# Kernel optimization log

Measured on AMD Instinct MI355X. Metric: run time of the kernel, lower is better.

The kernel has to match this reference:

```python
import jax, jax.numpy as jnp
import numpy as np

TEMPERATURE = 0.07
EPS = 1e-8  # torch CosineSimilarity eps default


def setup_inputs() -> dict:
    key = jax.random.key(0)
    k1, k2 = jax.random.split(key)
    N, D = 8192, 1024
    image_features = jax.random.normal(k1, (N, D), dtype=jnp.float32)
    text_features = jax.random.normal(k2, (N, D), dtype=jnp.float32)
    return {"image_features": image_features, "text_features": text_features}


def _normalize(x):
    # matches torch cosine similarity denominator clamp: norm >= eps
    n = jnp.sqrt(jnp.sum(x * x, axis=-1, keepdims=True))
    return x / jnp.maximum(n, EPS)


def reference(image_features, text_features):
    # cosine similarity via normalize + GEMM (same math as broadcasted NxNxD form)
    img_n = _normalize(image_features)  # [N, D]
    txt_n = _normalize(text_features)   # [N, D]
    logits = jnp.einsum('id,jd->ij', img_n, txt_n) / TEMPERATURE  # [N, N]

    N = logits.shape[0]
    labels = jnp.arange(N)
    # cross-entropy with labels = diagonal indices
    logp_i2t = jax.nn.log_softmax(logits, axis=-1)      # rows: image -> text
    logp_t2i = jax.nn.log_softmax(logits.T, axis=-1)    # rows: text -> image
    loss_i2t = -jnp.mean(logp_i2t[labels, labels])
    loss_t2i = -jnp.mean(logp_t2i[labels, labels])
    return (loss_i2t + loss_t2i) / 2
```

## Files before the change

### kernel.cpp

```cpp
#include <hip/hip_runtime.h>


#define BM 128
#define BN 128
#define BKB 128

typedef float floatx4 __attribute__((ext_vector_type(4)));
typedef int   intx4   __attribute__((ext_vector_type(4)));
typedef int   intx8   __attribute__((ext_vector_type(8)));

__device__ __forceinline__ void gload_lds16(const unsigned char* g, unsigned char* lds) {
    __builtin_amdgcn_global_load_lds(
        (const __attribute__((address_space(1))) void*)g,
        (__attribute__((address_space(3))) void*)lds,
        16, 0, 0);
}

__global__ __launch_bounds__(256)
void normalize_fp8(const float* __restrict__ img, const float* __restrict__ txt,
                   unsigned int* __restrict__ oimg, unsigned int* __restrict__ otxt,
                   float* __restrict__ sums, float* __restrict__ out, int N) {
    const int gi = blockIdx.x * 256 + threadIdx.x;
    if (gi < 2 * N) sums[gi] = 0.f;
    if (gi == 0) out[0] = 0.f;

    const int gw = blockIdx.x * 4 + (threadIdx.x >> 6);
    const int lane = threadIdx.x & 63;
    const float* in = (gw < N) ? img : txt;
    unsigned int* o = (gw < N) ? oimg : otxt;
    const int row = (gw < N) ? gw : gw - N;
    const float4* rp = (const float4*)(in + (size_t)row * 1024);

    float4 v[4];
    float ss = 0.f;
    #pragma unroll
    for (int j = 0; j < 4; ++j) {
        v[j] = rp[j * 64 + lane];
        ss += v[j].x * v[j].x + v[j].y * v[j].y + v[j].z * v[j].z + v[j].w * v[j].w;
    }
    #pragma unroll
    for (int o2 = 1; o2 < 64; o2 <<= 1) ss += __shfl_xor(ss, o2);
    const float inv = 16.0f / fmaxf(sqrtf(ss), 1e-8f);
    #pragma unroll
    for (int j = 0; j < 4; ++j) {
        int p = __builtin_amdgcn_cvt_pk_fp8_f32(v[j].x * inv, v[j].y * inv, 0, false);
        p = __builtin_amdgcn_cvt_pk_fp8_f32(v[j].z * inv, v[j].w * inv, p, true);
        const int d = j * 64 + lane;
        const int c = (d >> 2) & 7;
        const int pp = (c & 1) * 4 + (c >> 1);
        const int dp = (d & ~31) | (pp * 4 + (d & 3));
        o[(size_t)row * 256 + dp] = (unsigned int)p;
    }
}

__global__ __launch_bounds__(256)
void gemm_exp_kernel(const unsigned char* __restrict__ A,
                     const unsigned char* __restrict__ B,
                     float* __restrict__ rowsum, float* __restrict__ colsum,
                     float* __restrict__ diag, int K, float scale) {
    __shared__ unsigned char As[2 * BM * 64];
    __shared__ unsigned char Bs[2 * BN * 64];

    const int bm = blockIdx.x, bn = blockIdx.y;
    const int tid = threadIdx.x;
    const int lane = tid & 63;
    const int wave = tid >> 6;
    const int quad = lane >> 4;
    const int lanelo = lane & 15;
    const int wrow = (wave >> 1) * 64;
    const int wcol = (wave & 1) * 64;

    floatx4 acc[4][4] = {};

    const int c0 = wave * 128 + lane;
    const int c1 = c0 + 64;
    const int r0 = c0 >> 2, r1 = c1 >> 2;
    const int kg0 = ((c0 & 3) ^ ((r0 >> 1) & 3)) * 16;
    const int kg1 = ((c1 & 3) ^ ((r1 >> 1) & 3)) * 16;

    const unsigned char* pa0 = A + (size_t)bm * BM * K + (size_t)r0 * K + kg0;
    const unsigned char* pa1 = A + (size_t)bm * BM * K + (size_t)r1 * K + kg1;
    const unsigned char* pb0 = B + (size_t)bn * BN * K + (size_t)r0 * K + kg0;
    const unsigned char* pb1 = B + (size_t)bn * BN * K + (size_t)r1 * K + kg1;
    unsigned char* dA0 = As + c0 * 16;
    unsigned char* dA1 = As + c1 * 16;
    unsigned char* dB0 = Bs + c0 * 16;
    unsigned char* dB1 = Bs + c1 * 16;

    int aoff[4], boff[4];
    #pragma unroll
    for (int t = 0; t < 4; ++t) {
        const int Ra = wrow + t * 16 + lanelo;
        const int Rb = wcol + t * 16 + lanelo;
        aoff[t] = Ra * 64 + ((quad ^ ((Ra >> 1) & 3)) * 16);
        boff[t] = Rb * 64 + ((quad ^ ((Rb >> 1) & 3)) * 16);
    }

    for (int k0 = 0; k0 < K; k0 += BKB) {
        #pragma unroll
        for (int w = 0; w < 2; ++w) {
            gload_lds16(pa0 + w * 64, dA0 + w * 8192);
            gload_lds16(pa1 + w * 64, dA1 + w * 8192);
            gload_lds16(pb0 + w * 64, dB0 + w * 8192);
            gload_lds16(pb1 + w * 64, dB1 + w * 8192);
        }
        pa0 += BKB; pa1 += BKB; pb0 += BKB; pb1 += BKB;
        __syncthreads();

        intx8 af[4], bg[4];
        #pragma unroll
        for (int t = 0; t < 4; ++t) {
            const intx4 alo = *(const intx4*)(As + aoff[t]);
            const intx4 ahi = *(const intx4*)(As + 8192 + aoff[t]);
            af[t] = __builtin_shufflevector(alo, ahi, 0, 1, 2, 3, 4, 5, 6, 7);
            const intx4 blo = *(const intx4*)(Bs + boff[t]);
            const intx4 bhi = *(const intx4*)(Bs + 8192 + boff[t]);
            bg[t] = __builtin_shufflevector(blo, bhi, 0, 1, 2, 3, 4, 5, 6, 7);
        }

        #pragma unroll
        for (int tm = 0; tm < 4; ++tm)
            #pragma unroll
            for (int tn = 0; tn < 4; ++tn)
                acc[tm][tn] = __builtin_amdgcn_mfma_scale_f32_16x16x128_f8f6f4(
                    af[tm], bg[tn], acc[tm][tn],
                    0, 0,
                    0, 127,
                    0, 127);
        __syncthreads();
    }

    const int growb = bm * BM + wrow;
    const int gcolb = bn * BN + wcol;

    #pragma unroll
    for (int tm = 0; tm < 4; ++tm)
        #pragma unroll
        for (int tn = 0; tn < 4; ++tn)
            #pragma unroll
            for (int r = 0; r < 4; ++r) {
                const float l = acc[tm][tn][r] * scale;
                const int grow = growb + tm * 16 + quad * 4 + r;
                const int gcol = gcolb + tn * 16 + lanelo;
                if (grow == gcol) diag[grow] = l;
                acc[tm][tn][r] = __expf(l);
            }

    #pragma unroll
    for (int tm = 0; tm < 4; ++tm) {
        floatx4 rs = acc[tm][0] + acc[tm][1] + acc[tm][2] + acc[tm][3];
        #pragma unroll
        for (int r = 0; r < 4; ++r) {
            float v = rs[r];
            v += __shfl_xor(v, 1);
            v += __shfl_xor(v, 2);
            v += __shfl_xor(v, 4);
            v += __shfl_xor(v, 8);
            if (lanelo == 0)
                atomicAdd(&rowsum[growb + tm * 16 + quad * 4 + r], v);
        }
    }

    #pragma unroll
    for (int tn = 0; tn < 4; ++tn) {
        float cs = 0.f;
        #pragma unroll
        for (int tm = 0; tm < 4; ++tm)
            cs += acc[tm][tn][0] + acc[tm][tn][1] + acc[tm][tn][2] + acc[tm][tn][3];
        cs += __shfl_xor(cs, 16);
        cs += __shfl_xor(cs, 32);
        if (quad == 0)
            atomicAdd(&colsum[gcolb + tn * 16 + lanelo], cs);
    }
}

__global__ __launch_bounds__(256)
void final_reduce(const float* __restrict__ rowsum, const float* __restrict__ colsum,
                  const float* __restrict__ diag, float* __restrict__ out, int n) {
    const int i = blockIdx.x * 256 + threadIdx.x;
    const int t = threadIdx.x;
    float v = 0.5f * (logf(rowsum[i]) + logf(colsum[i])) - diag[i];
    #pragma unroll
    for (int o = 1; o < 64; o <<= 1) v += __shfl_xor(v, o);
    __shared__ float ws[4];
    if ((t & 63) == 0) ws[t >> 6] = v;
    __syncthreads();
    if (t == 0) atomicAdd(out, (ws[0] + ws[1] + ws[2] + ws[3]) / (float)n);
}

extern "C" void kernel_launch(void* const* d_in, const int* in_sizes, int n_in,
                              void* d_out, int out_size, void* d_ws, size_t ws_size,
                              hipStream_t stream) {
    const float* img = (const float*)d_in[0];
    const float* txt = (const float*)d_in[1];
    float* out = (float*)d_out;

    const int D = 1024;
    const int N = in_sizes[0] / D;

    unsigned char* imgq = (unsigned char*)d_ws;
    unsigned char* txtq = imgq + (size_t)N * D;
    float* rowsum = (float*)(txtq + (size_t)N * D);
    float* colsum = rowsum + N;
    float* diag = colsum + N;

    normalize_fp8<<<2 * N / 4, 256, 0, stream>>>(img, txt, (unsigned int*)imgq,
                                                 (unsigned int*)txtq, rowsum, out, N);

    dim3 grid(N / BM, N / BN);
    gemm_exp_kernel<<<grid, 256, 0, stream>>>(imgq, txtq, rowsum, colsum, diag,
                                              D, 1.0f / (256.0f * 0.07f));
    final_reduce<<<N / 256, 256, 0, stream>>>(rowsum, colsum, diag, out, N);
}
```

Baseline: 189.3 us.

## Double-buffer LDS tiles to overlap global loads with MFMA compute

Adds a second pair of shared-memory buffers and restructures the K loop so the next K-slice is issued via global_load_lds into the alternate buffer while the current buffer feeds the MFMAs. The goal is to hide global-memory latency that the single-buffered loop exposed between the two barriers. LDS use per block doubles to 64 KB, which may lower occupancy. The loop assumes K is a multiple of 2*BKB and relies on the barrier to wait for the async LDS loads.

```diff
diff --git a/kernel.cpp b/kernel.cpp
--- a/kernel.cpp
+++ b/kernel.cpp
@@ -58,8 +58,10 @@
                      const unsigned char* __restrict__ B,
                      float* __restrict__ rowsum, float* __restrict__ colsum,
                      float* __restrict__ diag, int K, float scale) {
-    __shared__ unsigned char As[2 * BM * 64];
-    __shared__ unsigned char Bs[2 * BN * 64];
+    __shared__ unsigned char As0[2 * BM * 64];
+    __shared__ unsigned char As1[2 * BM * 64];
+    __shared__ unsigned char Bs0[2 * BN * 64];
+    __shared__ unsigned char Bs1[2 * BN * 64];
 
     const int bm = blockIdx.x, bn = blockIdx.y;
     const int tid = threadIdx.x;
@@ -82,10 +84,8 @@
     const unsigned char* pa1 = A + (size_t)bm * BM * K + (size_t)r1 * K + kg1;
     const unsigned char* pb0 = B + (size_t)bn * BN * K + (size_t)r0 * K + kg0;
     const unsigned char* pb1 = B + (size_t)bn * BN * K + (size_t)r1 * K + kg1;
-    unsigned char* dA0 = As + c0 * 16;
-    unsigned char* dA1 = As + c1 * 16;
-    unsigned char* dB0 = Bs + c0 * 16;
-    unsigned char* dB1 = Bs + c1 * 16;
+    const int dofs0 = c0 * 16;
+    const int dofs1 = c1 * 16;
 
     int aoff[4], boff[4];
     #pragma unroll
@@ -96,28 +96,27 @@
         boff[t] = Rb * 64 + ((quad ^ ((Rb >> 1) & 3)) * 16);
     }
 
-    for (int k0 = 0; k0 < K; k0 += BKB) {
+    auto stage = [&](unsigned char* SA, unsigned char* SB, int k) {
         #pragma unroll
         for (int w = 0; w < 2; ++w) {
-            gload_lds16(pa0 + w * 64, dA0 + w * 8192);
-            gload_lds16(pa1 + w * 64, dA1 + w * 8192);
-            gload_lds16(pb0 + w * 64, dB0 + w * 8192);
-            gload_lds16(pb1 + w * 64, dB1 + w * 8192);
+            gload_lds16(pa0 + k + w * 64, SA + dofs0 + w * 8192);
+            gload_lds16(pa1 + k + w * 64, SA + dofs1 + w * 8192);
+            gload_lds16(pb0 + k + w * 64, SB + dofs0 + w * 8192);
+            gload_lds16(pb1 + k + w * 64, SB + dofs1 + w * 8192);
         }
-        pa0 += BKB; pa1 += BKB; pb0 += BKB; pb1 += BKB;
-        __syncthreads();
-
+    };
+
+    auto compute = [&](const unsigned char* SA, const unsigned char* SB) {
         intx8 af[4], bg[4];
         #pragma unroll
         for (int t = 0; t < 4; ++t) {
-            const intx4 alo = *(const intx4*)(As + aoff[t]);
-            const intx4 ahi = *(const intx4*)(As + 8192 + aoff[t]);
+            const intx4 alo = *(const intx4*)(SA + aoff[t]);
+            const intx4 ahi = *(const intx4*)(SA + 8192 + aoff[t]);
             af[t] = __builtin_shufflevector(alo, ahi, 0, 1, 2, 3, 4, 5, 6, 7);
-            const intx4 blo = *(const intx4*)(Bs + boff[t]);
-            const intx4 bhi = *(const intx4*)(Bs + 8192 + boff[t]);
+            const intx4 blo = *(const intx4*)(SB + boff[t]);
+            const intx4 bhi = *(const intx4*)(SB + 8192 + boff[t]);
             bg[t] = __builtin_shufflevector(blo, bhi, 0, 1, 2, 3, 4, 5, 6, 7);
         }
-
         #pragma unroll
         for (int tm = 0; tm < 4; ++tm)
             #pragma unroll
@@ -127,7 +126,16 @@
                     0, 0,
                     0, 127,
                     0, 127);
+    };
+
+    stage(As0, Bs0, 0);
+    for (int k = 0; k < K; k += 2 * BKB) {
         __syncthreads();
+        if (k + BKB < K) stage(As1, Bs1, k + BKB);
+        compute(As0, Bs0);
+        __syncthreads();
+        if (k + 2 * BKB < K) stage(As0, Bs0, k + 2 * BKB);
+        compute(As1, Bs1);
     }
 
     const int growb = bm * BM + wrow;
```

Result: slower. 202.1 us (+6.8%).
